# Kernel tuning notes

Measured on AMD Instinct MI355X. Metric: run time of the kernel, lower is better.

## Reference

```python
import jax, jax.numpy as jnp
import numpy as np

N_DELTA, N_THETA, N_GAMMA = 2, 4, 8
N_OSC = N_DELTA + N_THETA + N_GAMMA  # 14
INPUT_DIM = 512
N_CLASSES = 2
COUPLING = 1.5
DT = 0.01
N_STEPS = 100


def _natural_freqs():
    # Natural frequencies (Hz) per EEG band: delta ~2Hz, theta ~6Hz, gamma ~40Hz
    return jnp.concatenate([
        jnp.full((N_DELTA,), 2.0, dtype=jnp.float32),
        jnp.full((N_THETA,), 6.0, dtype=jnp.float32),
        jnp.full((N_GAMMA,), 40.0, dtype=jnp.float32),
    ])


def setup_inputs() -> dict:
    key = jax.random.key(0)
    k_x, k_win, k_wc = jax.random.split(key, 3)
    x = jax.random.normal(k_x, (4096, 64, INPUT_DIM), dtype=jnp.float32)
    W_in = jax.random.normal(k_win, (INPUT_DIM, N_OSC), dtype=jnp.float32) / np.sqrt(INPUT_DIM)
    b_in = jnp.zeros((N_OSC,), dtype=jnp.float32)
    omega = _natural_freqs()
    Wc = jax.random.normal(k_wc, (N_OSC, N_CLASSES), dtype=jnp.float32) / np.sqrt(N_OSC)
    bc = jnp.zeros((N_CLASSES,), dtype=jnp.float32)
    return {"x": x, "W_in": W_in, "b_in": b_in, "omega": omega, "Wc": Wc, "bc": bc}


def reference(x, W_in, b_in, omega, Wc, bc):
    # Mean-pool over the object/token dimension: [B,S,D] -> [B,D]
    if x.ndim == 3:
        x = x.mean(axis=1)
    # Project input features to initial oscillator phases: [B,14]
    theta0 = x @ W_in + b_in
    two_pi = jnp.float32(2.0 * np.pi)
    k_over_n = jnp.float32(COUPLING / N_OSC)
    dt = jnp.float32(DT)

    def step(theta, _):
        s = jnp.sin(theta)
        c = jnp.cos(theta)
        # mean-field Kuramoto coupling: sum_j sin(th_j - th_i) = S*cos(th_i) - C*sin(th_i)
        S = s.sum(axis=-1, keepdims=True)
        C = c.sum(axis=-1, keepdims=True)
        dtheta = two_pi * omega + k_over_n * (S * c - C * s)
        return theta + dt * dtheta, None

    theta, _ = jax.lax.scan(step, theta0, None, length=N_STEPS)
    h = jnp.cos(theta)  # oscillator readout: [B,14]
    logits = h @ Wc + bc
    return jax.nn.log_softmax(logits, axis=-1)
```

## Files before the change

### kernel.cpp

```cpp
#include <hip/hip_runtime.h>
#include <math.h>

#define SEQ   64
#define DIM   512
#define NOSC  14
#define NSTEP 100
#define RPB   4

typedef float f4 __attribute__((ext_vector_type(4)));

__device__ __forceinline__ float dpp_sum16(float v) {
    v += __int_as_float(__builtin_amdgcn_update_dpp(0, __float_as_int(v), 0xB1,  0xF, 0xF, true));
    v += __int_as_float(__builtin_amdgcn_update_dpp(0, __float_as_int(v), 0x4E,  0xF, 0xF, true));
    v += __int_as_float(__builtin_amdgcn_update_dpp(0, __float_as_int(v), 0x141, 0xF, 0xF, true));
    v += __int_as_float(__builtin_amdgcn_update_dpp(0, __float_as_int(v), 0x140, 0xF, 0xF, true));
    return v;
}

__device__ __forceinline__ void fast_sincos(float theta, float* s, float* c) {
    const float inv2pi = 0.15915494309189535f;
    float r = theta * inv2pi;
    r = r - floorf(r);
    *s = __builtin_amdgcn_sinf(r);
    *c = __builtin_amdgcn_cosf(r);
}

__global__ __launch_bounds__(256, 4)
void fused_kernel(const float* __restrict__ x,
                  const float* __restrict__ W_in,
                  const float* __restrict__ b_in,
                  const float* __restrict__ omega,
                  const float* __restrict__ Wc,
                  const float* __restrict__ bc,
                  float* __restrict__ out, int B)
{
    const int t    = threadIdx.x;
    const int row0 = blockIdx.x * RPB;

    __shared__ f4    mv[2][DIM / 4];
    __shared__ float pp[NOSC][16];

    if (t < 128 && row0 < B) {
        const f4* xv = reinterpret_cast<const f4*>(x + (size_t)row0 * (SEQ * DIM));
        f4 acc = (f4)(0.0f);
#pragma unroll 8
        for (int s = 0; s < SEQ; ++s)
            acc += __builtin_nontemporal_load(&xv[s * (DIM / 4) + t]);
        mv[0][t] = acc * (1.0f / SEQ);
    }
    __syncthreads();
    {
        const float* m = reinterpret_cast<const float*>(mv[0]);
        if (t < NOSC * 16) {
            const int o  = t >> 4;
            const int ch = t & 15;
            float p = 0.f;
#pragma unroll 8
            for (int i = 0; i < 32; ++i) {
                const int d = i * 16 + ch;
                p += m[d] * W_in[d * NOSC + o];
            }
            pp[o][ch] = p;
        }
    }
    __syncthreads();

    for (int r = 0; r < RPB; ++r) {
        const int nb = (r & 1) ^ 1;
        if (t >= 192) {
            const int lane = t - 192;
            const int row  = row0 + r;
            if (lane < 16 && row < B) {
                const bool  act  = (lane < NOSC);
                const float mask = act ? 1.0f : 0.0f;
                const int   oc   = act ? lane : (NOSC - 1);

                float theta = 0.0f;
                if (act) {
                    theta = b_in[lane];
#pragma unroll
                    for (int ch = 0; ch < 16; ++ch) theta += pp[lane][ch];
                }
                const float drift = 6.283185307179586f * omega[oc];
                const float kn = 1.5f / (float)NOSC;
                const float dt = 0.01f;

                for (int it = 0; it < NSTEP; ++it) {
                    float s_, c_;
                    fast_sincos(theta, &s_, &c_);
                    s_ *= mask; c_ *= mask;
                    const float S = dpp_sum16(s_);
                    const float C = dpp_sum16(c_);
                    theta += dt * (drift + kn * (S * c_ - C * s_));
                }

                float hs, hc;
                fast_sincos(theta, &hs, &hc);
                const float h = hc * mask;
                float z0 = dpp_sum16(h * Wc[oc * 2 + 0]);
                float z1 = dpp_sum16(h * Wc[oc * 2 + 1]);
                if (lane == 0) {
                    z0 += bc[0]; z1 += bc[1];
                    const float mx  = fmaxf(z0, z1);
                    const float lse = mx + logf(expf(z0 - mx) + expf(z1 - mx));
                    out[(size_t)row * 2 + 0] = z0 - lse;
                    out[(size_t)row * 2 + 1] = z1 - lse;
                }
            }
        } else if (t < 128 && r + 1 < RPB && row0 + r + 1 < B) {
            const f4* xv = reinterpret_cast<const f4*>(x + (size_t)(row0 + r + 1) * (SEQ * DIM));
            f4 acc = (f4)(0.0f);
#pragma unroll 8
            for (int s = 0; s < SEQ; ++s)
                acc += __builtin_nontemporal_load(&xv[s * (DIM / 4) + t]);
            mv[nb][t] = acc * (1.0f / SEQ);
        }
        __syncthreads();
        if (r + 1 < RPB) {
            const float* m = reinterpret_cast<const float*>(mv[nb]);
            if (t < NOSC * 16) {
                const int o  = t >> 4;
                const int ch = t & 15;
                float p = 0.f;
#pragma unroll 8
                for (int i = 0; i < 32; ++i) {
                    const int d = i * 16 + ch;
                    p += m[d] * W_in[d * NOSC + o];
                }
                pp[o][ch] = p;
            }
        }
        __syncthreads();
    }
}

extern "C" void kernel_launch(void* const* d_in, const int* in_sizes, int n_in,
                              void* d_out, int out_size, void* d_ws, size_t ws_size,
                              hipStream_t stream)
{
    const float* x     = (const float*)d_in[0];
    const float* W_in  = (const float*)d_in[1];
    const float* b_in  = (const float*)d_in[2];
    const float* omega = (const float*)d_in[3];
    const float* Wc    = (const float*)d_in[4];
    const float* bc    = (const float*)d_in[5];
    float* out = (float*)d_out;

    const int B = in_sizes[0] / (SEQ * DIM);

    const int grid = (B + RPB - 1) / RPB;
    fused_kernel<<<grid, 256, 0, stream>>>(x, W_in, b_in, omega, Wc, bc, out, B);
}
```

Measured before the change: 98.34 us.

## Use flag-synchronized producer/consumer waves and batch oscillator integration across rows

Replaces the barrier-separated per-row pipeline with two loader waves that each pool and project two rows, publishing initial phases through LDS with release flags. A single consumer wave spins on the flags and integrates all four rows concurrently, 16 lanes per row. The aim is to remove block-wide barriers and to overlap or shorten the serial Kuramoto tail. It adds spin-waiting and relies on workgroup-scope atomic ordering.

```diff
diff --git a/kernel.cpp b/kernel.cpp
--- a/kernel.cpp
+++ b/kernel.cpp
@@ -9,6 +9,11 @@
 
 typedef float f4 __attribute__((ext_vector_type(4)));
 
+__device__ __forceinline__ float dpp_sum4(float v) {
+    v += __int_as_float(__builtin_amdgcn_update_dpp(0, __float_as_int(v), 0xB1,  0xF, 0xF, true));
+    v += __int_as_float(__builtin_amdgcn_update_dpp(0, __float_as_int(v), 0x4E,  0xF, 0xF, true));
+    return v;
+}
 __device__ __forceinline__ float dpp_sum16(float v) {
     v += __int_as_float(__builtin_amdgcn_update_dpp(0, __float_as_int(v), 0xB1,  0xF, 0xF, true));
     v += __int_as_float(__builtin_amdgcn_update_dpp(0, __float_as_int(v), 0x4E,  0xF, 0xF, true));
@@ -35,102 +40,90 @@
                   float* __restrict__ out, int B)
 {
     const int t    = threadIdx.x;
+    const int wv   = t >> 6;
+    const int ln   = t & 63;
     const int row0 = blockIdx.x * RPB;
 
-    __shared__ f4    mv[2][DIM / 4];
-    __shared__ float pp[NOSC][16];
+    __shared__ f4    mvbuf[2][2][DIM / 4];
+    __shared__ float th0[RPB][16];
+    __shared__ int   flags[RPB];
 
-    if (t < 128 && row0 < B) {
-        const f4* xv = reinterpret_cast<const f4*>(x + (size_t)row0 * (SEQ * DIM));
-        f4 acc = (f4)(0.0f);
-#pragma unroll 8
-        for (int s = 0; s < SEQ; ++s)
-            acc += __builtin_nontemporal_load(&xv[s * (DIM / 4) + t]);
-        mv[0][t] = acc * (1.0f / SEQ);
-    }
-    __syncthreads();
-    {
-        const float* m = reinterpret_cast<const float*>(mv[0]);
-        if (t < NOSC * 16) {
-            const int o  = t >> 4;
-            const int ch = t & 15;
-            float p = 0.f;
-#pragma unroll 8
-            for (int i = 0; i < 32; ++i) {
-                const int d = i * 16 + ch;
-                p += m[d] * W_in[d * NOSC + o];
-            }
-            pp[o][ch] = p;
-        }
-    }
+    if (t < RPB) flags[t] = 0;
     __syncthreads();
 
-    for (int r = 0; r < RPB; ++r) {
-        const int nb = (r & 1) ^ 1;
-        if (t >= 192) {
-            const int lane = t - 192;
-            const int row  = row0 + r;
-            if (lane < 16 && row < B) {
-                const bool  act  = (lane < NOSC);
-                const float mask = act ? 1.0f : 0.0f;
-                const int   oc   = act ? lane : (NOSC - 1);
+    if (wv < 2) {
+        const int o = ln >> 2;
+        const int q = ln & 3;
+        for (int rr = 0; rr < RPB / 2; ++rr) {
+            const int r   = wv + 2 * rr;
+            const int row = row0 + r;
+            if (row >= B) break;
 
-                float theta = 0.0f;
-                if (act) {
-                    theta = b_in[lane];
-#pragma unroll
-                    for (int ch = 0; ch < 16; ++ch) theta += pp[lane][ch];
-                }
-                const float drift = 6.283185307179586f * omega[oc];
-                const float kn = 1.5f / (float)NOSC;
-                const float dt = 0.01f;
+            const f4* xv = reinterpret_cast<const f4*>(x + (size_t)row * (SEQ * DIM));
+            f4 a0 = (f4)(0.0f), a1 = (f4)(0.0f);
+#pragma unroll 8
+            for (int s = 0; s < SEQ; ++s) {
+                a0 += __builtin_nontemporal_load(&xv[s * (DIM / 4) + ln]);
+                a1 += __builtin_nontemporal_load(&xv[s * (DIM / 4) + 64 + ln]);
+            }
+            f4* mw = mvbuf[wv][rr & 1];
+            mw[ln]      = a0 * (1.0f / SEQ);
+            mw[ln + 64] = a1 * (1.0f / SEQ);
+            asm volatile("s_waitcnt lgkmcnt(0)" ::: "memory");
 
-                for (int it = 0; it < NSTEP; ++it) {
-                    float s_, c_;
-                    fast_sincos(theta, &s_, &c_);
-                    s_ *= mask; c_ *= mask;
-                    const float S = dpp_sum16(s_);
-                    const float C = dpp_sum16(c_);
-                    theta += dt * (drift + kn * (S * c_ - C * s_));
-                }
-
-                float hs, hc;
-                fast_sincos(theta, &hs, &hc);
-                const float h = hc * mask;
-                float z0 = dpp_sum16(h * Wc[oc * 2 + 0]);
-                float z1 = dpp_sum16(h * Wc[oc * 2 + 1]);
-                if (lane == 0) {
-                    z0 += bc[0]; z1 += bc[1];
-                    const float mx  = fmaxf(z0, z1);
-                    const float lse = mx + logf(expf(z0 - mx) + expf(z1 - mx));
-                    out[(size_t)row * 2 + 0] = z0 - lse;
-                    out[(size_t)row * 2 + 1] = z1 - lse;
+            const float* m = reinterpret_cast<const float*>(mw);
+            float p = 0.f;
+            if (o < NOSC) {
+#pragma unroll 16
+                for (int i = 0; i < 128; ++i) {
+                    const int d = q * 128 + i;
+                    p += m[d] * W_in[d * NOSC + o];
                 }
             }
-        } else if (t < 128 && r + 1 < RPB && row0 + r + 1 < B) {
-            const f4* xv = reinterpret_cast<const f4*>(x + (size_t)(row0 + r + 1) * (SEQ * DIM));
-            f4 acc = (f4)(0.0f);
-#pragma unroll 8
-            for (int s = 0; s < SEQ; ++s)
-                acc += __builtin_nontemporal_load(&xv[s * (DIM / 4) + t]);
-            mv[nb][t] = acc * (1.0f / SEQ);
+            p = dpp_sum4(p);
+            if (q == 0) th0[r][o] = (o < NOSC) ? (p + b_in[o]) : 0.f;
+            if (ln == 0)
+                __hip_atomic_store(&flags[r], 1, __ATOMIC_RELEASE, __HIP_MEMORY_SCOPE_WORKGROUP);
         }
-        __syncthreads();
-        if (r + 1 < RPB) {
-            const float* m = reinterpret_cast<const float*>(mv[nb]);
-            if (t < NOSC * 16) {
-                const int o  = t >> 4;
-                const int ch = t & 15;
-                float p = 0.f;
-#pragma unroll 8
-                for (int i = 0; i < 32; ++i) {
-                    const int d = i * 16 + ch;
-                    p += m[d] * W_in[d * NOSC + o];
-                }
-                pp[o][ch] = p;
+    } else if (wv == 3) {
+        const int grp = ln >> 4;
+        const int o   = ln & 15;
+        const int row = row0 + grp;
+        if (row < B) {
+            while (__hip_atomic_load(&flags[grp], __ATOMIC_ACQUIRE, __HIP_MEMORY_SCOPE_WORKGROUP) == 0)
+                __builtin_amdgcn_s_sleep(4);
+
+            const bool  act  = (o < NOSC);
+            const float mask = act ? 1.0f : 0.0f;
+            const int   oc   = act ? o : (NOSC - 1);
+
+            float theta = th0[grp][o];
+            const float drift = 6.283185307179586f * omega[oc];
+            const float kn = 1.5f / (float)NOSC;
+            const float dt = 0.01f;
+
+            for (int it = 0; it < NSTEP; ++it) {
+                float s_, c_;
+                fast_sincos(theta, &s_, &c_);
+                s_ *= mask; c_ *= mask;
+                const float S = dpp_sum16(s_);
+                const float C = dpp_sum16(c_);
+                theta += dt * (drift + kn * (S * c_ - C * s_));
+            }
+
+            float hs, hc;
+            fast_sincos(theta, &hs, &hc);
+            const float h = hc * mask;
+            float z0 = dpp_sum16(h * Wc[oc * 2 + 0]);
+            float z1 = dpp_sum16(h * Wc[oc * 2 + 1]);
+            if (o == 0) {
+                z0 += bc[0]; z1 += bc[1];
+                const float mx  = fmaxf(z0, z1);
+                const float lse = mx + logf(expf(z0 - mx) + expf(z1 - mx));
+                out[(size_t)row * 2 + 0] = z0 - lse;
+                out[(size_t)row * 2 + 1] = z1 - lse;
             }
         }
-        __syncthreads();
     }
 }
 
```

New measurement: 99.69 us. About the same (+1.4%).
